# Kernel tuning notes

Measured on AMD Instinct MI355X. Metric: run time of the kernel, lower is better.

Reference implementation:

```python
import jax, jax.numpy as jnp
import numpy as np

NX = NY = 2048
DT = 0.01
DX = 1.0
DY = 1.0
RE = 1.0
NLEVEL = int(np.log2(NY)) + 1  # 12 levels


def pad_zero(x):
    # Dirichlet (zero) halo of width 1: matches boundary_condition_u/v/k/cw
    return jnp.pad(x, ((0, 0), (0, 0), (1, 1), (1, 1)))


def pad_edge(x):
    # Edge-replicate halo (incl. corners): matches boundary_condition_p
    return jnp.pad(x, ((0, 0), (0, 0), (1, 1), (1, 1)), mode='edge')


def conv2d(x, w, stride=1):
    return jax.lax.conv_general_dilated(
        x, w, (stride, stride), 'VALID',
        dimension_numbers=('NCHW', 'OIHW', 'NCHW'))


def upsample2(x):
    return jnp.repeat(jnp.repeat(x, 2, axis=2), 2, axis=3)


def pg_vector(u, v, pad_u, pad_v, k1, ADx_u, ADy_u, ADx_v, ADy_v, AD2_u, AD2_v, w_diff):
    # Petrov-Galerkin dissipation. pad_u/pad_v are the padded ORIGINAL velocities:
    # the torch code references the global values_uu/values_vv buffers here.
    k_u = 0.25 * DX * jnp.abs(0.5 * DX ** -3 * (jnp.abs(u) * DX + jnp.abs(v) * DY) * AD2_u) \
        / (0.001 + (jnp.abs(ADx_u) * DX ** -3 + jnp.abs(ADy_u) * DX ** -3) / 2.0)
    k_v = 0.25 * DY * jnp.abs(0.5 * DX ** -3 * (jnp.abs(u) * DX + jnp.abs(v) * DY) * AD2_v) \
        / (0.001 + (jnp.abs(ADx_v) * DX ** -3 + jnp.abs(ADy_v) * DX ** -3) / 2.0)
    k_u = jnp.minimum(k_u, k1)
    k_v = jnp.minimum(k_v, k1)
    k_uu = pad_zero(k_u)
    k_vv = pad_zero(k_v)
    k_x = 1.5 * (k_u * AD2_u + conv2d(pad_u * k_uu, w_diff) - u * conv2d(k_uu, w_diff))
    k_y = 1.5 * (k_v * AD2_v + conv2d(pad_v * k_vv, w_diff) - v * conv2d(k_vv, w_diff))
    return k_x, k_y


def f_cycle_mg(pad_u, pad_v, values_p, iteration, w_A, w_res, w_xadv, w_yadv):
    diag = w_A[0, 0, 1, 1]
    b = -(conv2d(pad_u, w_xadv) + conv2d(pad_v, w_yadv)) / DT
    w = jnp.zeros((1, 1, 2, 2), values_p.dtype)
    r = b
    for _ in range(iteration):
        w = jnp.zeros((1, 1, 2, 2), values_p.dtype)
        r = conv2d(pad_edge(values_p), w_A) - b
        r_s = [r]
        for _i in range(1, NLEVEL - 1):
            r = conv2d(r, w_res, stride=2)  # restriction down to 2x2
            r_s.append(r)
        for i in reversed(range(1, NLEVEL - 1)):
            w = w - conv2d(pad_zero(w), w_A) / diag + r_s[i] / diag  # Jacobi smooth
            w = upsample2(w)  # prolongation
        values_p = values_p - w
        values_p = values_p - conv2d(pad_edge(values_p), w_A) / diag + b / diag
    return values_p, w, r


def setup_inputs() -> dict:
    key = jax.random.key(0)
    ku, kv, kp = jax.random.split(key, 3)
    shp = (1, 1, NY, NX)
    f32 = jnp.float32
    values_u = jax.random.normal(ku, shp, f32) * 0.1
    values_v = jax.random.normal(kv, shp, f32) * 0.1
    values_p = jax.random.normal(kp, shp, f32) * 0.1
    Fx = jnp.zeros(shp, f32)
    Fy = jnp.zeros(shp, f32)
    k1 = jnp.ones(shp, f32) * (DX ** 2 / DT)
    # FD stencils (learned conv params in the torch module)
    w_xadv = jnp.array([[0., 0., 0.], [-0.5, 0., 0.5], [0., 0., 0.]], f32).reshape(1, 1, 3, 3) / DX
    w_yadv = jnp.array([[0., -0.5, 0.], [0., 0., 0.], [0., 0.5, 0.]], f32).reshape(1, 1, 3, 3) / DY
    lap = jnp.array([[0., 1., 0.], [1., -4., 1.], [0., 1., 0.]], f32).reshape(1, 1, 3, 3) / DX ** 2
    w_diff = lap
    w_A = lap  # diag = -4
    w_res = jnp.full((1, 1, 2, 2), 0.25, f32)
    return dict(values_u=values_u, values_v=values_v, values_p=values_p,
                Fx=Fx, Fy=Fy, k1=k1,
                w_xadv=w_xadv, w_yadv=w_yadv, w_diff=w_diff, w_A=w_A, w_res=w_res,
                iteration=5)


def reference(values_u, values_v, values_p, Fx, Fy, k1,
              w_xadv, w_yadv, w_diff, w_A, w_res, iteration):
    pad_u = pad_zero(values_u)
    pad_v = pad_zero(values_v)
    pad_p = pad_edge(values_p)
    Grapx_p = conv2d(pad_p, w_xadv) * DT
    Grapy_p = conv2d(pad_p, w_yadv) * DT
    ADx_u = conv2d(pad_u, w_xadv); ADy_u = conv2d(pad_u, w_yadv)
    ADx_v = conv2d(pad_v, w_xadv); ADy_v = conv2d(pad_v, w_yadv)
    AD2_u = conv2d(pad_u, w_diff); AD2_v = conv2d(pad_v, w_diff)
    k_x, k_y = pg_vector(values_u, values_v, pad_u, pad_v, k1,
                         ADx_u, ADy_u, ADx_v, ADy_v, AD2_u, AD2_v, w_diff)
    b_u = values_u + 0.5 * (RE * k_x * DT - values_u * ADx_u * DT - values_v * ADy_u * DT) - Grapx_p - Fx * DT * 0
    b_v = values_v + 0.5 * (RE * k_y * DT - values_u * ADx_v * DT - values_v * ADy_v * DT) - Grapy_p - Fy * DT * 0
    pad_bu = pad_zero(b_u)
    pad_bv = pad_zero(b_v)
    ADx_u = conv2d(pad_bu, w_xadv); ADy_u = conv2d(pad_bu, w_yadv)
    ADx_v = conv2d(pad_bv, w_xadv); ADy_v = conv2d(pad_bv, w_yadv)
    AD2_u = conv2d(pad_bu, w_diff); AD2_v = conv2d(pad_bv, w_diff)
    # torch code closes over the global padded ORIGINAL velocities here (pad_u, pad_v)
    k_x, k_y = pg_vector(b_u, b_v, pad_u, pad_v, k1,
                         ADx_u, ADy_u, ADx_v, ADy_v, AD2_u, AD2_v, w_diff)
    values_u = values_u + RE * k_x * DT - b_u * ADx_u * DT - b_v * ADy_u * DT - Grapx_p - Fx * DT
    values_v = values_v + RE * k_y * DT - b_u * ADx_v * DT - b_v * ADy_v * DT - Grapy_p - Fy * DT
    values_p, w, r = f_cycle_mg(pad_zero(values_u), pad_zero(values_v), values_p,
                                iteration, w_A, w_res, w_xadv, w_yadv)
    pad_p2 = pad_edge(values_p)
    values_u = values_u - conv2d(pad_p2, w_xadv) * DT
    values_v = values_v - conv2d(pad_p2, w_yadv) * DT
    return values_u, values_v, values_p, w, r
```

## Files before the change

### kernel.cpp

```cpp
#include <hip/hip_runtime.h>

#define NN 2048
#define NN2 (NN * NN)

__device__ __forceinline__ void load6z(const float* __restrict__ A, int i, int j0, float a[6]) {
    if ((unsigned)i >= (unsigned)NN) {
#pragma unroll
        for (int q = 0; q < 6; ++q) a[q] = 0.f;
        return;
    }
    const float* row = A + (size_t)i * NN;
    float4 c = *reinterpret_cast<const float4*>(row + j0);
    a[1] = c.x; a[2] = c.y; a[3] = c.z; a[4] = c.w;
    a[0] = (j0 > 0) ? row[j0 - 1] : 0.f;
    a[5] = (j0 + 4 < NN) ? row[j0 + 4] : 0.f;
}
__device__ __forceinline__ void load4z(const float* __restrict__ A, int i, int j0, float a[4]) {
    if ((unsigned)i >= (unsigned)NN) {
#pragma unroll
        for (int q = 0; q < 4; ++q) a[q] = 0.f;
        return;
    }
    float4 c = *reinterpret_cast<const float4*>(A + (size_t)i * NN + j0);
    a[0] = c.x; a[1] = c.y; a[2] = c.z; a[3] = c.w;
}
__device__ __forceinline__ void load6e(const float* __restrict__ A, int i, int j0, float a[6]) {
    i = i < 0 ? 0 : (i > NN - 1 ? NN - 1 : i);
    const float* row = A + (size_t)i * NN;
    float4 c = *reinterpret_cast<const float4*>(row + j0);
    a[1] = c.x; a[2] = c.y; a[3] = c.z; a[4] = c.w;
    a[0] = (j0 > 0) ? row[j0 - 1] : c.x;
    a[5] = (j0 + 4 < NN) ? row[j0 + 4] : c.w;
}
__device__ __forceinline__ void load4e(const float* __restrict__ A, int i, int j0, float a[4]) {
    i = i < 0 ? 0 : (i > NN - 1 ? NN - 1 : i);
    float4 c = *reinterpret_cast<const float4*>(A + (size_t)i * NN + j0);
    a[0] = c.x; a[1] = c.y; a[2] = c.z; a[3] = c.w;
}
__device__ __forceinline__ void store4(float* __restrict__ A, int i, int j0, const float a[4]) {
    *reinterpret_cast<float4*>(A + (size_t)i * NN + j0) = make_float4(a[0], a[1], a[2], a[3]);
}

__global__ __launch_bounds__(256) void k_pred_f(const float* __restrict__ u, const float* __restrict__ v,
                                                const float* __restrict__ k1, const float* __restrict__ p,
                                                float* __restrict__ bu, float* __restrict__ bv) {
    const float DT = 0.01f;
    __shared__ __align__(16) float su[20][72], sv[20][72];
    __shared__ float sku[18][68], skv[18][68];
    const int jb = blockIdx.x * 64;
    const int ib = blockIdx.y * 16;
    const int tid = threadIdx.y * 16 + threadIdx.x;

    for (int idx = tid; idx < 20 * 18; idx += 256) {
        int r = idx / 18, c4 = idx - r * 18;
        int gi = ib - 2 + r;
        int gj = jb - 4 + c4 * 4;
        float4 uu = make_float4(0.f, 0.f, 0.f, 0.f), vv = uu;
        if ((unsigned)gi < (unsigned)NN) {
            if (gj >= 0 && gj + 3 < NN) {
                uu = *reinterpret_cast<const float4*>(u + (size_t)gi * NN + gj);
                vv = *reinterpret_cast<const float4*>(v + (size_t)gi * NN + gj);
            } else {
                float tu[4], tv[4];
#pragma unroll
                for (int q = 0; q < 4; ++q) {
                    int g = gj + q;
                    bool in = (unsigned)g < (unsigned)NN;
                    tu[q] = in ? u[(size_t)gi * NN + g] : 0.f;
                    tv[q] = in ? v[(size_t)gi * NN + g] : 0.f;
                }
                uu = make_float4(tu[0], tu[1], tu[2], tu[3]);
                vv = make_float4(tv[0], tv[1], tv[2], tv[3]);
            }
        }
        *reinterpret_cast<float4*>(&su[r][c4 * 4]) = uu;
        *reinterpret_cast<float4*>(&sv[r][c4 * 4]) = vv;
    }
    __syncthreads();

    for (int idx = tid; idx < 18 * 66; idx += 256) {
        int r = idx / 66, c = idx - r * 66;
        int gi = ib - 1 + r, gj = jb - 1 + c;
        float kuo = 0.f, kvo = 0.f;
        if ((unsigned)gi < (unsigned)NN && (unsigned)gj < (unsigned)NN) {
            int lr = r + 1, lc = c + 3;
            float uc = su[lr][lc], ul = su[lr][lc - 1], ur = su[lr][lc + 1], ut = su[lr - 1][lc], ub = su[lr + 1][lc];
            float vc = sv[lr][lc], vl = sv[lr][lc - 1], vr = sv[lr][lc + 1], vt = sv[lr - 1][lc], vb = sv[lr + 1][lc];
            float ADxu = 0.5f * (ur - ul), ADyu = 0.5f * (ub - ut);
            float ADxv = 0.5f * (vr - vl), ADyv = 0.5f * (vb - vt);
            float Lu = ul + ur + ut + ub - 4.f * uc;
            float Lv = vl + vr + vt + vb - 4.f * vc;
            float s = fabsf(uc) + fabsf(vc);
            float kuv = 0.25f * fabsf(0.5f * s * Lu) / (0.001f + 0.5f * (fabsf(ADxu) + fabsf(ADyu)));
            float kvv = 0.25f * fabsf(0.5f * s * Lv) / (0.001f + 0.5f * (fabsf(ADxv) + fabsf(ADyv)));
            float k1c = k1[(size_t)gi * NN + gj];
            kuo = fminf(kuv, k1c);
            kvo = fminf(kvv, k1c);
        }
        sku[r][c] = kuo;
        skv[r][c] = kvo;
    }
    __syncthreads();

    const int i = ib + threadIdx.y;
    const int j0 = jb + threadIdx.x * 4;
    float p6[6], pu[4], pd[4], obu[4], obv[4];
    load6e(p, i, j0, p6); load4e(p, i - 1, j0, pu); load4e(p, i + 1, j0, pd);
    const int lur = threadIdx.y + 2, lkr = threadIdx.y + 1;
#pragma unroll
    for (int c = 0; c < 4; ++c) {
        int luc = threadIdx.x * 4 + c + 4, lkc = threadIdx.x * 4 + c + 1;
        float uc = su[lur][luc], ul = su[lur][luc - 1], ur = su[lur][luc + 1], ut = su[lur - 1][luc], ub = su[lur + 1][luc];
        float vc = sv[lur][luc], vl = sv[lur][luc - 1], vr = sv[lur][luc + 1], vt = sv[lur - 1][luc], vb = sv[lur + 1][luc];
        float kuc = sku[lkr][lkc], kul = sku[lkr][lkc - 1], kur = sku[lkr][lkc + 1], kut = sku[lkr - 1][lkc], kub = sku[lkr + 1][lkc];
        float kvc = skv[lkr][lkc], kvl = skv[lkr][lkc - 1], kvr = skv[lkr][lkc + 1], kvt = skv[lkr - 1][lkc], kvb = skv[lkr + 1][lkc];
        float ADxu = 0.5f * (ur - ul), ADyu = 0.5f * (ub - ut);
        float ADxv = 0.5f * (vr - vl), ADyv = 0.5f * (vb - vt);
        float Lu = ul + ur + ut + ub - 4.f * uc;
        float Lv = vl + vr + vt + vb - 4.f * vc;
        float Lku = kul + kur + kut + kub - 4.f * kuc;
        float Lkv = kvl + kvr + kvt + kvb - 4.f * kvc;
        float Luku = ul * kul + ur * kur + ut * kut + ub * kub - 4.f * uc * kuc;
        float Lvkv = vl * kvl + vr * kvr + vt * kvt + vb * kvb - 4.f * vc * kvc;
        float kx = 1.5f * (kuc * Lu + Luku - uc * Lku);
        float ky = 1.5f * (kvc * Lv + Lvkv - vc * Lkv);
        float Grapx = 0.5f * (p6[c + 2] - p6[c]) * DT;
        float Grapy = 0.5f * (pd[c] - pu[c]) * DT;
        obu[c] = uc + 0.5f * (kx * DT - uc * ADxu * DT - vc * ADyu * DT) - Grapx;
        obv[c] = vc + 0.5f * (ky * DT - uc * ADxv * DT - vc * ADyv * DT) - Grapy;
    }
    store4(bu, i, j0, obu);
    store4(bv, i, j0, obv);
}

__global__ __launch_bounds__(256) void k_corr_f(const float* __restrict__ u, const float* __restrict__ v,
                                                const float* __restrict__ k1, const float* __restrict__ p,
                                                const float* __restrict__ bu, const float* __restrict__ bv,
                                                const float* __restrict__ Fx, const float* __restrict__ Fy,
                                                float* __restrict__ un, float* __restrict__ vn) {
    const float DT = 0.01f;
    __shared__ __align__(16) float sbu[20][72], sbv[20][72];
    __shared__ float sku[18][68], skv[18][68];
    const int jb = blockIdx.x * 64;
    const int ib = blockIdx.y * 16;
    const int tid = threadIdx.y * 16 + threadIdx.x;

    for (int idx = tid; idx < 20 * 18; idx += 256) {
        int r = idx / 18, c4 = idx - r * 18;
        int gi = ib - 2 + r;
        int gj = jb - 4 + c4 * 4;
        float4 uu = make_float4(0.f, 0.f, 0.f, 0.f), vv = uu;
        if ((unsigned)gi < (unsigned)NN) {
            if (gj >= 0 && gj + 3 < NN) {
                uu = *reinterpret_cast<const float4*>(bu + (size_t)gi * NN + gj);
                vv = *reinterpret_cast<const float4*>(bv + (size_t)gi * NN + gj);
            } else {
                float tu[4], tv[4];
#pragma unroll
                for (int q = 0; q < 4; ++q) {
                    int g = gj + q;
                    bool in = (unsigned)g < (unsigned)NN;
                    tu[q] = in ? bu[(size_t)gi * NN + g] : 0.f;
                    tv[q] = in ? bv[(size_t)gi * NN + g] : 0.f;
                }
                uu = make_float4(tu[0], tu[1], tu[2], tu[3]);
                vv = make_float4(tv[0], tv[1], tv[2], tv[3]);
            }
        }
        *reinterpret_cast<float4*>(&sbu[r][c4 * 4]) = uu;
        *reinterpret_cast<float4*>(&sbv[r][c4 * 4]) = vv;
    }
    __syncthreads();

    for (int idx = tid; idx < 18 * 66; idx += 256) {
        int r = idx / 66, c = idx - r * 66;
        int gi = ib - 1 + r, gj = jb - 1 + c;
        float kuo = 0.f, kvo = 0.f;
        if ((unsigned)gi < (unsigned)NN && (unsigned)gj < (unsigned)NN) {
            int lr = r + 1, lc = c + 3;
            float uc = sbu[lr][lc], ul = sbu[lr][lc - 1], ur = sbu[lr][lc + 1], ut = sbu[lr - 1][lc], ub = sbu[lr + 1][lc];
            float vc = sbv[lr][lc], vl = sbv[lr][lc - 1], vr = sbv[lr][lc + 1], vt = sbv[lr - 1][lc], vb = sbv[lr + 1][lc];
            float ADxu = 0.5f * (ur - ul), ADyu = 0.5f * (ub - ut);
            float ADxv = 0.5f * (vr - vl), ADyv = 0.5f * (vb - vt);
            float Lu = ul + ur + ut + ub - 4.f * uc;
            float Lv = vl + vr + vt + vb - 4.f * vc;
            float s = fabsf(uc) + fabsf(vc);
            float kuv = 0.25f * fabsf(0.5f * s * Lu) / (0.001f + 0.5f * (fabsf(ADxu) + fabsf(ADyu)));
            float kvv = 0.25f * fabsf(0.5f * s * Lv) / (0.001f + 0.5f * (fabsf(ADxv) + fabsf(ADyv)));
            float k1c = k1[(size_t)gi * NN + gj];
            kuo = fminf(kuv, k1c);
            kvo = fminf(kvv, k1c);
        }
        sku[r][c] = kuo;
        skv[r][c] = kvo;
    }
    __syncthreads();

    const int i = ib + threadIdx.y;
    const int j0 = jb + threadIdx.x * 4;
    float p6[6], pu[4], pd[4];
    float u6[6], uu[4], ud[4], v6[6], vu[4], vd[4], fx[4], fy[4], oun[4], ovn[4];
    load6e(p, i, j0, p6); load4e(p, i - 1, j0, pu); load4e(p, i + 1, j0, pd);
    load6z(u, i, j0, u6); load4z(u, i - 1, j0, uu); load4z(u, i + 1, j0, ud);
    load6z(v, i, j0, v6); load4z(v, i - 1, j0, vu); load4z(v, i + 1, j0, vd);
    load4z(Fx, i, j0, fx); load4z(Fy, i, j0, fy);
    const int lbr = threadIdx.y + 2, lkr = threadIdx.y + 1;
#pragma unroll
    for (int c = 0; c < 4; ++c) {
        int lbc = threadIdx.x * 4 + c + 4, lkc = threadIdx.x * 4 + c + 1;
        float buc = sbu[lbr][lbc], bul = sbu[lbr][lbc - 1], bur = sbu[lbr][lbc + 1], but = sbu[lbr - 1][lbc], bub = sbu[lbr + 1][lbc];
        float bvc = sbv[lbr][lbc], bvl = sbv[lbr][lbc - 1], bvr = sbv[lbr][lbc + 1], bvt = sbv[lbr - 1][lbc], bvb = sbv[lbr + 1][lbc];
        float kuc = sku[lkr][lkc], kul = sku[lkr][lkc - 1], kur = sku[lkr][lkc + 1], kut = sku[lkr - 1][lkc], kub = sku[lkr + 1][lkc];
        float kvc = skv[lkr][lkc], kvl = skv[lkr][lkc - 1], kvr = skv[lkr][lkc + 1], kvt = skv[lkr - 1][lkc], kvb = skv[lkr + 1][lkc];
        float uc = u6[c + 1], ul = u6[c], ur = u6[c + 2], ut = uu[c], ub = ud[c];
        float vc = v6[c + 1], vl = v6[c], vr = v6[c + 2], vt = vu[c], vb = vd[c];
        float ADxbu = 0.5f * (bur - bul), ADybu = 0.5f * (bub - but);
        float ADxbv = 0.5f * (bvr - bvl), ADybv = 0.5f * (bvb - bvt);
        float Lbu = bul + bur + but + bub - 4.f * buc;
        float Lbv = bvl + bvr + bvt + bvb - 4.f * bvc;
        float Lku = kul + kur + kut + kub - 4.f * kuc;
        float Lkv = kvl + kvr + kvt + kvb - 4.f * kvc;
        float Luku = ul * kul + ur * kur + ut * kut + ub * kub - 4.f * uc * kuc;
        float Lvkv = vl * kvl + vr * kvr + vt * kvt + vb * kvb - 4.f * vc * kvc;
        float kx = 1.5f * (kuc * Lbu + Luku - buc * Lku);
        float ky = 1.5f * (kvc * Lbv + Lvkv - bvc * Lkv);
        float Grapx = 0.5f * (p6[c + 2] - p6[c]) * DT;
        float Grapy = 0.5f * (pd[c] - pu[c]) * DT;
        oun[c] = uc + kx * DT - buc * ADxbu * DT - bvc * ADybu * DT - Grapx - fx[c] * DT;
        ovn[c] = vc + ky * DT - buc * ADxbv * DT - bvc * ADybv * DT - Grapy - fy[c] * DT;
    }
    store4(un, i, j0, oun);
    store4(vn, i, j0, ovn);
}

__global__ __launch_bounds__(256) void k_rhs_res(const float* __restrict__ un, const float* __restrict__ vn,
                                                 const float* __restrict__ p, float* __restrict__ b,
                                                 float* __restrict__ r1024, float* __restrict__ r512,
                                                 float* __restrict__ r256) {
    __shared__ float s512r[4][64];
    int tx = threadIdx.x, ty = threadIdx.y;
    int jt = blockIdx.x * 64 + tx;
    int it = blockIdx.y * 4 + ty;
    int j0 = jt * 4, i0 = it * 4;
    float bb[4][4];
#pragma unroll
    for (int r = 0; r < 4; ++r) {
        float u6[6], vu[4], vd[4];
        load6z(un, i0 + r, j0, u6);
        load4z(vn, i0 + r - 1, j0, vu);
        load4z(vn, i0 + r + 1, j0, vd);
#pragma unroll
        for (int c = 0; c < 4; ++c)
            bb[r][c] = -100.f * (0.5f * (u6[c + 2] - u6[c]) + 0.5f * (vd[c] - vu[c]));
        store4(b, i0 + r, j0, bb[r]);
    }
    float p6[6][6];
#pragma unroll
    for (int r = 0; r < 6; ++r) load6e(p, i0 - 1 + r, j0, p6[r]);
    float res[4][4];
#pragma unroll
    for (int r = 0; r < 4; ++r)
#pragma unroll
        for (int c = 0; c < 4; ++c) {
            float pc = p6[r + 1][c + 1];
            res[r][c] = p6[r][c + 1] + p6[r + 2][c + 1] + p6[r + 1][c] + p6[r + 1][c + 2] - 4.f * pc - bb[r][c];
        }
    float q00 = 0.25f * (res[0][0] + res[0][1] + res[1][0] + res[1][1]);
    float q01 = 0.25f * (res[0][2] + res[0][3] + res[1][2] + res[1][3]);
    float q10 = 0.25f * (res[2][0] + res[2][1] + res[3][0] + res[3][1]);
    float q11 = 0.25f * (res[2][2] + res[2][3] + res[3][2] + res[3][3]);
    int ci = it * 2, cj = jt * 2;
    *reinterpret_cast<float2*>(r1024 + (size_t)ci * 1024 + cj)       = make_float2(q00, q01);
    *reinterpret_cast<float2*>(r1024 + (size_t)(ci + 1) * 1024 + cj) = make_float2(q10, q11);
    float s = 0.25f * (q00 + q01 + q10 + q11);
    r512[(size_t)it * 512 + jt] = s;
    s512r[ty][tx] = s;
    __syncthreads();
    int tid = ty * 64 + tx;
    if (tid < 64) {
        int a = tid >> 5, c = tid & 31;
        float m = 0.25f * (s512r[2 * a][2 * c] + s512r[2 * a][2 * c + 1] + s512r[2 * a + 1][2 * c] + s512r[2 * a + 1][2 * c + 1]);
        r256[(size_t)(blockIdx.y * 2 + a) * 256 + blockIdx.x * 32 + c] = m;
    }
}

__global__ __launch_bounds__(1024) void k_small2(const float* __restrict__ r256in,
                                                 float* __restrict__ r128g,
                                                 float* __restrict__ w128_out,
                                                 float* __restrict__ r2_out) {
    __shared__ float sr128[128 * 128];
    __shared__ float sr64[64 * 64];
    __shared__ float sr32[32 * 32];
// ... 32 lines not shown
    }
    __syncthreads();
    if (t < 64) {
        int i = t >> 3, j = t & 7;
        const float* s0 = sr16 + (2 * i) * 16 + 2 * j;
        sr8[t] = 0.25f * (s0[0] + s0[1] + s0[16] + s0[17]);
    }
    __syncthreads();
    if (t < 16) {
        int i = t >> 2, j = t & 3;
        const float* s0 = sr8 + (2 * i) * 8 + 2 * j;
        sr4[t] = 0.25f * (s0[0] + s0[1] + s0[8] + s0[9]);
    }
    __syncthreads();
    if (t < 4) {
        int i = t >> 1, j = t & 1;
        const float* s0 = sr4 + (2 * i) * 4 + 2 * j;
        sr2[t] = 0.25f * (s0[0] + s0[1] + s0[4] + s0[5]);
        r2_out[t] = sr2[t];
        float ws = -0.25f * sr2[t];
        wa[(2 * i) * 4 + 2 * j] = ws;
        wa[(2 * i) * 4 + 2 * j + 1] = ws;
        wa[(2 * i + 1) * 4 + 2 * j] = ws;
        wa[(2 * i + 1) * 4 + 2 * j + 1] = ws;
    }
    __syncthreads();

    auto step = [&](const float* win, const float* rl, float* wout, int s) {
        for (int idx = t; idx < s * s; idx += 1024) {
            int i = idx / s, j = idx - i * s;
            float up = i > 0 ? win[(i - 1) * s + j] : 0.f;
            float dn = i < s - 1 ? win[(i + 1) * s + j] : 0.f;
            float lf = j > 0 ? win[i * s + j - 1] : 0.f;
            float rt = j < s - 1 ? win[i * s + j + 1] : 0.f;
            float ws = 0.25f * (up + dn + lf + rt - rl[idx]);
            int o = 2 * s;
            wout[(2 * i) * o + 2 * j] = ws;
            wout[(2 * i) * o + 2 * j + 1] = ws;
            wout[(2 * i + 1) * o + 2 * j] = ws;
            wout[(2 * i + 1) * o + 2 * j + 1] = ws;
        }
    };
    step(wa, sr4, wb, 4);
    __syncthreads();
    step(wb, sr8, wa, 8);
    __syncthreads();
    step(wa, sr16, wb, 16);
    __syncthreads();
    step(wb, sr32, wa, 32);
    __syncthreads();
    step(wa, sr64, w128_out, 64);
}

__global__ __launch_bounds__(256) void k_prolong2(const float* __restrict__ w128, const float* __restrict__ r128,
                                                  const float* __restrict__ r256, float* __restrict__ w512) {
    __shared__ float sw[5][68];
    __shared__ float s128[3][66];
    __shared__ float s256[2][128];
    const int jb = blockIdx.x * 256;
    const int ob = blockIdx.y * 4;
    const int by = blockIdx.y;
    const int rw = by - 2, cw = jb / 4 - 2;
    const int rs = by - 1, cs = jb / 4 - 1;
    const int tid = threadIdx.y * 64 + threadIdx.x;

    for (int idx = tid; idx < 5 * 68; idx += 256) {
        int r = idx / 68, c = idx - r * 68;
        int x = rw + r, y = cw + c;
        sw[r][c] = ((unsigned)x < 128u && (unsigned)y < 128u) ? w128[x * 128 + y] : 0.f;
    }
    __syncthreads();
    if (tid < 3 * 66) {
        int r = tid / 66, c = tid - (tid / 66) * 66;
        int x = rs + r, y = cs + c;
        float val = 0.f;
        if ((unsigned)x < 128u && (unsigned)y < 128u) {
            int lr = r + 1, lc = c + 1;
            val = 0.25f * (sw[lr - 1][lc] + sw[lr + 1][lc] + sw[lr][lc - 1] + sw[lr][lc + 1] - r128[x * 128 + y]);
        }
        s128[r][c] = val;
    }
    __syncthreads();
    {
        int rr = tid >> 7, cc = tid & 127;
        int X = 2 * by + rr, Y = jb / 2 + cc;
        float s = 0.f;
        if (X > 0)   s += s128[((X - 1) >> 1) - rs][(Y >> 1) - cs];
        if (X < 255) s += s128[((X + 1) >> 1) - rs][(Y >> 1) - cs];
        if (Y > 0)   s += s128[(X >> 1) - rs][((Y - 1) >> 1) - cs];
        if (Y < 255) s += s128[(X >> 1) - rs][((Y + 1) >> 1) - cs];
        s256[rr][cc] = 0.25f * (s - r256[X * 256 + Y]);
    }
    __syncthreads();
    const int i = ob + threadIdx.y;
    const int j0 = jb + threadIdx.x * 4;
    const int lr = (i >> 1) - 2 * by;
    float o[4];
#pragma unroll
    for (int c = 0; c < 4; ++c) o[c] = s256[lr][((j0 + c) >> 1) - jb / 2];
    *reinterpret_cast<float4*>(w512 + (size_t)i * 512 + j0) = make_float4(o[0], o[1], o[2], o[3]);
}

template <bool LAST>
__global__ __launch_bounds__(256) void k_pupd3(
    const float* __restrict__ p, const float* __restrict__ b,
    const float* __restrict__ w512, const float* __restrict__ r512,
    const float* __restrict__ r1024,
    float* __restrict__ pdst,
    float* __restrict__ o1024, float* __restrict__ o512, float* __restrict__ o256,
    float* __restrict__ wout, float* __restrict__ un, float* __restrict__ vn)
{
    __shared__ float sW[6][38];
    __shared__ float sS[4][36];
    __shared__ float ws[6][68];
    __shared__ __align__(16) float pmid[12][136];
    __shared__ float pnew[10][130];
    __shared__ float sq[4][64];
    __shared__ float red[2][32];

    const int jb = blockIdx.x * 128;
    const int ib = blockIdx.y * 8;
    const int tid = threadIdx.y * 32 + threadIdx.x;
    const int r1 = ib / 2 - 1, c1 = jb / 2 - 2;
    const int r2 = ib / 4 - 1, c2 = jb / 4 - 2;
    const int r3 = ib / 4 - 2, c3 = jb / 4 - 3;

    for (int idx = tid; idx < 6 * 38; idx += 256) {
        int r = idx / 38, c = idx - r * 38;
        int x = r3 + r, y = c3 + c;
        sW[r][c] = ((unsigned)x < 512u && (unsigned)y < 512u) ? w512[(size_t)x * 512 + y] : 0.f;
    }
    __syncthreads();
    if (tid < 4 * 36) {
        int r = tid / 36, c = tid - (tid / 36) * 36;
        int x = r2 + r, y = c2 + c;
        float val = 0.f;
        if ((unsigned)x < 512u && (unsigned)y < 512u) {
            int lr = r + 1, lc = c + 1;
            val = 0.25f * (sW[lr - 1][lc] + sW[lr + 1][lc] + sW[lr][lc - 1] + sW[lr][lc + 1]
                           - r512[(size_t)x * 512 + y]);
        }
        sS[r][c] = val;
    }
    __syncthreads();
    for (int idx = tid; idx < 6 * 68; idx += 256) {
        int r = idx / 68, c = idx - r * 68;
        int x = r1 + r, y = c1 + c;
        float val = 0.f;
        if ((unsigned)x < 1024u && (unsigned)y < 1024u) {
            float s = 0.f;
            if (x > 0)    s += sS[((x - 1) >> 1) - r2][(y >> 1) - c2];
            if (x < 1023) s += sS[((x + 1) >> 1) - r2][(y >> 1) - c2];
            if (y > 0)    s += sS[(x >> 1) - r2][((y - 1) >> 1) - c2];
            if (y < 1023) s += sS[(x >> 1) - r2][((y + 1) >> 1) - c2];
            val = 0.25f * (s - r1024[(size_t)x * 1024 + y]);
        }
        ws[r][c] = val;
    }
    __syncthreads();
    for (int idx = tid; idx < 12 * 34; idx += 256) {
        int r = idx / 34, q = idx - r * 34;
        int gi = ib - 2 + r;
        int gj0 = jb - 4 + q * 4;
        float vals[4] = {0.f, 0.f, 0.f, 0.f};
        if ((unsigned)gi < (unsigned)NN) {
            if (gj0 >= 0 && gj0 + 3 < NN) {
                float4 pv = *reinterpret_cast<const float4*>(p + (size_t)gi * NN + gj0);
                vals[0] = pv.x; vals[1] = pv.y; vals[2] = pv.z; vals[3] = pv.w;
            } else {
#pragma unroll
                for (int q4 = 0; q4 < 4; ++q4) {
                    int gj = gj0 + q4;
                    vals[q4] = ((unsigned)gj < (unsigned)NN) ? p[(size_t)gi * NN + gj] : 0.f;
                }
            }
        }
#pragma unroll
        for (int q4 = 0; q4 < 4; ++q4) {
            int gj = gj0 + q4;
            float m = 0.f;
            if ((unsigned)gi < (unsigned)NN && (unsigned)gj < (unsigned)NN &&
                gj >= jb - 2 && gj <= jb + 129) {
                m = vals[q4] - ws[(gi >> 1) - r1][(gj >> 1) - c1];
            }
            pmid[r][q * 4 + q4] = m;
        }
    }
    __syncthreads();
    for (int idx = tid; idx < 10 * 130; idx += 256) {
        int r = idx / 130, c = idx - r * 130;
        int gi = ib - 1 + r, gj = jb - 1 + c;
        float val = 0.f;
        if ((unsigned)gi < (unsigned)NN && (unsigned)gj < (unsigned)NN) {
// ... 12 lines not shown
    const int i  = ib + threadIdx.y;
    const int j0 = jb + threadIdx.x * 4;
    const int lr = i - (ib - 1);
    const int lc = j0 - (jb - 1);
    *reinterpret_cast<float4*>(pdst + (size_t)i * NN + j0) =
        make_float4(pnew[lr][lc], pnew[lr][lc + 1], pnew[lr][lc + 2], pnew[lr][lc + 3]);

    if (LAST) {
        const float DT = 0.01f;
        float ow[4];
        int wr = (i >> 1) - r1;
#pragma unroll
        for (int c = 0; c < 4; ++c) ow[c] = ws[wr][((j0 + c) >> 1) - c1];
        store4(wout, i, j0, ow);
        float4 uu = *reinterpret_cast<float4*>(un + (size_t)i * NN + j0);
        float4 vv = *reinterpret_cast<float4*>(vn + (size_t)i * NN + j0);
        float ou[4] = {uu.x, uu.y, uu.z, uu.w};
        float ov[4] = {vv.x, vv.y, vv.z, vv.w};
        int iu = (i > 0 ? i - 1 : 0) - (ib - 1);
        int idn = (i < NN - 1 ? i + 1 : NN - 1) - (ib - 1);
#pragma unroll
        for (int c = 0; c < 4; ++c) {
            int j = j0 + c;
            int jl = (j > 0 ? j - 1 : 0) - (jb - 1);
            int jr = (j < NN - 1 ? j + 1 : NN - 1) - (jb - 1);
            int lcc = j - (jb - 1);
            ou[c] -= 0.5f * (pnew[lr][jr] - pnew[lr][jl]) * DT;
            ov[c] -= 0.5f * (pnew[idn][lcc] - pnew[iu][lcc]) * DT;
        }
        store4(un, i, j0, ou);
        store4(vn, i, j0, ov);
    } else {
        int cr = tid >> 6, cc = tid & 63;
        float q = 0.f;
#pragma unroll
        for (int dr = 0; dr < 2; ++dr) {
#pragma unroll
            for (int dc = 0; dc < 2; ++dc) {
                int i2 = ib + 2 * cr + dr, j2 = jb + 2 * cc + dc;
                int lr2 = i2 - (ib - 1), lc2 = j2 - (jb - 1);
                int iu2 = (i2 > 0 ? i2 - 1 : 0) - (ib - 1);
                int id2 = (i2 < NN - 1 ? i2 + 1 : NN - 1) - (ib - 1);
                int jl2 = (j2 > 0 ? j2 - 1 : 0) - (jb - 1);
                int jr2 = (j2 < NN - 1 ? j2 + 1 : NN - 1) - (jb - 1);
                q += pnew[iu2][lc2] + pnew[id2][lc2] + pnew[lr2][jl2] + pnew[lr2][jr2]
                   - 4.f * pnew[lr2][lc2] - b[(size_t)i2 * NN + j2];
            }
        }
        q *= 0.25f;
        sq[cr][cc] = q;
        o1024[(size_t)(ib / 2 + cr) * 1024 + jb / 2 + cc] = q;
        __syncthreads();
        if (tid < 64) {
            int rr = tid >> 5, c5 = tid & 31;
            float m = 0.25f * (sq[2 * rr][2 * c5] + sq[2 * rr][2 * c5 + 1] +
                               sq[2 * rr + 1][2 * c5] + sq[2 * rr + 1][2 * c5 + 1]);
            o512[(size_t)(ib / 4 + rr) * 512 + jb / 4 + c5] = m;
            red[rr][c5] = m;
        }
        __syncthreads();
        if (tid < 16) {
            float m = 0.25f * (red[0][2 * tid] + red[0][2 * tid + 1] +
                               red[1][2 * tid] + red[1][2 * tid + 1]);
            o256[(size_t)(ib / 8) * 256 + jb / 8 + tid] = m;
        }
    }
}

extern "C" void kernel_launch(void* const* d_in, const int* in_sizes, int n_in,
                              void* d_out, int out_size, void* d_ws, size_t ws_size,
                              hipStream_t stream) {
    const float* u  = (const float*)d_in[0];
    const float* v  = (const float*)d_in[1];
    const float* p  = (const float*)d_in[2];
    const float* Fx = (const float*)d_in[3];
    const float* Fy = (const float*)d_in[4];
    const float* k1 = (const float*)d_in[5];

    float* out = (float*)d_out;
    float* out_u = out;
    float* out_v = out + (size_t)NN2;
    float* out_p = out + 2 * (size_t)NN2;
    float* out_w = out + 3 * (size_t)NN2;
    float* out_r = out + 4 * (size_t)NN2;

    float* wsb = (float*)d_ws;
    float* b  = wsb;
    float* pA = wsb + (size_t)NN2;
    float* pB = wsb + 2 * (size_t)NN2;
    float* base = wsb + 3 * (size_t)NN2;
    float* rA1024 = base;
    float* rA512  = rA1024 + 1024 * 1024;
    float* rA256  = rA512 + 512 * 512;
    float* rB1024 = rA256 + 256 * 256;
    float* rB512  = rB1024 + 1024 * 1024;
    float* rB256  = rB512 + 512 * 512;
    float* r128   = rB256 + 256 * 256;
    float* w128   = r128 + 128 * 128;
    float* w512   = w128 + 128 * 128;

    float* bu = out_w;
    float* bv = out_p;

    dim3 blkT(16, 16);
    dim3 gT(32, 128);
    dim3 blkR(64, 4);
    dim3 gR(8, 128);
    dim3 blkP(32, 8);
    dim3 gP(16, 256);
    dim3 gL(2, 128);

    k_pred_f<<<gT, blkT, 0, stream>>>(u, v, k1, p, bu, bv);
    k_corr_f<<<gT, blkT, 0, stream>>>(u, v, k1, p, bu, bv, Fx, Fy, out_u, out_v);
    k_rhs_res<<<gR, blkR, 0, stream>>>(out_u, out_v, p, b, rA1024, rA512, rA256);

    const float* pcur = p;
    for (int it = 0; it < 5; ++it) {
        const bool useA = (it % 2 == 0);
        const float* R1024 = useA ? rA1024 : rB1024;
        const float* R512  = useA ? rA512  : rB512;
        const float* R256  = useA ? rA256  : rB256;
        float* O1024 = useA ? rB1024 : rA1024;
        float* O512  = useA ? rB512  : rA512;
        float* O256  = useA ? rB256  : rA256;

        k_small2<<<1, 1024, 0, stream>>>(R256, r128, w128, out_r);
        k_prolong2<<<gL, blkR, 0, stream>>>(w128, r128, R256, w512);
        if (it < 4) {
            float* pdst = (it & 1) ? pB : pA;
            k_pupd3<false><<<gP, blkP, 0, stream>>>(pcur, b, w512, R512, R1024,
                                                    pdst, O1024, O512, O256,
                                                    nullptr, nullptr, nullptr);
            pcur = pdst;
        } else {
            k_pupd3<true><<<gP, blkP, 0, stream>>>(pcur, b, w512, R512, R1024,
                                                   out_p, nullptr, nullptr, nullptr,
                                                   out_w, out_u, out_v);
        }
    }
}
```

Measured before the change: 393.1 us.

## Fuse momentum predictor/corrector and fold prolongation into pressure update kernel

Merges the predictor and corrector kernels into one kernel. It recomputes the intermediate b_u/b_v and the k fields on a wider halo in shared memory, so the intermediate no longer makes a global round trip. It also removes the separate 128→256→512 prolongation kernel: each pressure-update block now rebuilds its own w512 tile from w128, r128 and r256 locally. This cuts launches per multigrid iteration and global traffic, at the cost of redundant halo computation, more shared memory per block (possibly lower occupancy), and a few extra barriers. Shared arrays are also padded by one column to reduce bank conflicts.

```diff
diff --git a/kernel.cpp b/kernel.cpp
--- a/kernel.cpp
+++ b/kernel.cpp
@@ -32,58 +32,77 @@
     a[0] = (j0 > 0) ? row[j0 - 1] : c.x;
     a[5] = (j0 + 4 < NN) ? row[j0 + 4] : c.w;
 }
-__device__ __forceinline__ void load4e(const float* __restrict__ A, int i, int j0, float a[4]) {
-    i = i < 0 ? 0 : (i > NN - 1 ? NN - 1 : i);
-    float4 c = *reinterpret_cast<const float4*>(A + (size_t)i * NN + j0);
-    a[0] = c.x; a[1] = c.y; a[2] = c.z; a[3] = c.w;
-}
 __device__ __forceinline__ void store4(float* __restrict__ A, int i, int j0, const float a[4]) {
     *reinterpret_cast<float4*>(A + (size_t)i * NN + j0) = make_float4(a[0], a[1], a[2], a[3]);
 }
 
-__global__ __launch_bounds__(256) void k_pred_f(const float* __restrict__ u, const float* __restrict__ v,
-                                                const float* __restrict__ k1, const float* __restrict__ p,
-                                                float* __restrict__ bu, float* __restrict__ bv) {
+__global__ __launch_bounds__(256) void k_mom(const float* __restrict__ u, const float* __restrict__ v,
+                                             const float* __restrict__ k1, const float* __restrict__ p,
+                                             const float* __restrict__ Fx, const float* __restrict__ Fy,
+                                             float* __restrict__ un, float* __restrict__ vn) {
     const float DT = 0.01f;
-    __shared__ __align__(16) float su[20][72], sv[20][72];
-    __shared__ float sku[18][68], skv[18][68];
+    __shared__ float su[24][73], sv[24][73];
+    __shared__ float sp[22][73];
+    __shared__ float sku[22][71], skv[22][71];
+    __shared__ float sbu[20][69], sbv[20][69];
+    __shared__ float skbu[18][67], skbv[18][67];
     const int jb = blockIdx.x * 64;
     const int ib = blockIdx.y * 16;
     const int tid = threadIdx.y * 16 + threadIdx.x;
 
-    for (int idx = tid; idx < 20 * 18; idx += 256) {
+    for (int idx = tid; idx < 24 * 18; idx += 256) {
         int r = idx / 18, c4 = idx - r * 18;
-        int gi = ib - 2 + r;
+        int gi = ib - 4 + r;
         int gj = jb - 4 + c4 * 4;
-        float4 uu = make_float4(0.f, 0.f, 0.f, 0.f), vv = uu;
+        float tu[4] = {0.f, 0.f, 0.f, 0.f}, tv[4] = {0.f, 0.f, 0.f, 0.f};
         if ((unsigned)gi < (unsigned)NN) {
             if (gj >= 0 && gj + 3 < NN) {
-                uu = *reinterpret_cast<const float4*>(u + (size_t)gi * NN + gj);
-                vv = *reinterpret_cast<const float4*>(v + (size_t)gi * NN + gj);
+                float4 a = *reinterpret_cast<const float4*>(u + (size_t)gi * NN + gj);
+                float4 bq = *reinterpret_cast<const float4*>(v + (size_t)gi * NN + gj);
+                tu[0] = a.x; tu[1] = a.y; tu[2] = a.z; tu[3] = a.w;
+                tv[0] = bq.x; tv[1] = bq.y; tv[2] = bq.z; tv[3] = bq.w;
             } else {
-                float tu[4], tv[4];
 #pragma unroll
                 for (int q = 0; q < 4; ++q) {
                     int g = gj + q;
-                    bool in = (unsigned)g < (unsigned)NN;
-                    tu[q] = in ? u[(size_t)gi * NN + g] : 0.f;
-                    tv[q] = in ? v[(size_t)gi * NN + g] : 0.f;
+                    if ((unsigned)g < (unsigned)NN) {
+                        tu[q] = u[(size_t)gi * NN + g];
+                        tv[q] = v[(size_t)gi * NN + g];
+                    }
                 }
-                uu = make_float4(tu[0], tu[1], tu[2], tu[3]);
-                vv = make_float4(tv[0], tv[1], tv[2], tv[3]);
             }
         }
-        *reinterpret_cast<float4*>(&su[r][c4 * 4]) = uu;
-        *reinterpret_cast<float4*>(&sv[r][c4 * 4]) = vv;
-    }
-    __syncthreads();
-
-    for (int idx = tid; idx < 18 * 66; idx += 256) {
-        int r = idx / 66, c = idx - r * 66;
-        int gi = ib - 1 + r, gj = jb - 1 + c;
+#pragma unroll
+        for (int q = 0; q < 4; ++q) { su[r][c4 * 4 + q] = tu[q]; sv[r][c4 * 4 + q] = tv[q]; }
+    }
+    for (int idx = tid; idx < 22 * 18; idx += 256) {
+        int r = idx / 18, c4 = idx - r * 18;
+        int gi = ib - 3 + r;
+        gi = gi < 0 ? 0 : (gi > NN - 1 ? NN - 1 : gi);
+        int gj = jb - 4 + c4 * 4;
+        float tp[4];
+        if (gj >= 0 && gj + 3 < NN) {
+            float4 a = *reinterpret_cast<const float4*>(p + (size_t)gi * NN + gj);
+            tp[0] = a.x; tp[1] = a.y; tp[2] = a.z; tp[3] = a.w;
+        } else {
+#pragma unroll
+            for (int q = 0; q < 4; ++q) {
+                int g = gj + q;
+                g = g < 0 ? 0 : (g > NN - 1 ? NN - 1 : g);
+                tp[q] = p[(size_t)gi * NN + g];
+            }
+        }
+#pragma unroll
+        for (int q = 0; q < 4; ++q) sp[r][c4 * 4 + q] = tp[q];
+    }
+    __syncthreads();
+
+    for (int idx = tid; idx < 22 * 70; idx += 256) {
+        int r = idx / 70, c = idx - r * 70;
+        int gi = ib - 3 + r, gj = jb - 3 + c;
         float kuo = 0.f, kvo = 0.f;
         if ((unsigned)gi < (unsigned)NN && (unsigned)gj < (unsigned)NN) {
-            int lr = r + 1, lc = c + 3;
+            int lr = r + 1, lc = c + 1;
             float uc = su[lr][lc], ul = su[lr][lc - 1], ur = su[lr][lc + 1], ut = su[lr - 1][lc], ub = su[lr + 1][lc];
             float vc = sv[lr][lc], vl = sv[lr][lc - 1], vr = sv[lr][lc + 1], vt = sv[lr - 1][lc], vb = sv[lr + 1][lc];
             float ADxu = 0.5f * (ur - ul), ADyu = 0.5f * (ub - ut);
@@ -102,73 +121,35 @@
     }
     __syncthreads();
 
-    const int i = ib + threadIdx.y;
-    const int j0 = jb + threadIdx.x * 4;
-    float p6[6], pu[4], pd[4], obu[4], obv[4];
-    load6e(p, i, j0, p6); load4e(p, i - 1, j0, pu); load4e(p, i + 1, j0, pd);
-    const int lur = threadIdx.y + 2, lkr = threadIdx.y + 1;
-#pragma unroll
-    for (int c = 0; c < 4; ++c) {
-        int luc = threadIdx.x * 4 + c + 4, lkc = threadIdx.x * 4 + c + 1;
-        float uc = su[lur][luc], ul = su[lur][luc - 1], ur = su[lur][luc + 1], ut = su[lur - 1][luc], ub = su[lur + 1][luc];
-        float vc = sv[lur][luc], vl = sv[lur][luc - 1], vr = sv[lur][luc + 1], vt = sv[lur - 1][luc], vb = sv[lur + 1][luc];
-        float kuc = sku[lkr][lkc], kul = sku[lkr][lkc - 1], kur = sku[lkr][lkc + 1], kut = sku[lkr - 1][lkc], kub = sku[lkr + 1][lkc];
-        float kvc = skv[lkr][lkc], kvl = skv[lkr][lkc - 1], kvr = skv[lkr][lkc + 1], kvt = skv[lkr - 1][lkc], kvb = skv[lkr + 1][lkc];
-        float ADxu = 0.5f * (ur - ul), ADyu = 0.5f * (ub - ut);
-        float ADxv = 0.5f * (vr - vl), ADyv = 0.5f * (vb - vt);
-        float Lu = ul + ur + ut + ub - 4.f * uc;
-        float Lv = vl + vr + vt + vb - 4.f * vc;
-        float Lku = kul + kur + kut + kub - 4.f * kuc;
-        float Lkv = kvl + kvr + kvt + kvb - 4.f * kvc;
-        float Luku = ul * kul + ur * kur + ut * kut + ub * kub - 4.f * uc * kuc;
-        float Lvkv = vl * kvl + vr * kvr + vt * kvt + vb * kvb - 4.f * vc * kvc;
-        float kx = 1.5f * (kuc * Lu + Luku - uc * Lku);
-        float ky = 1.5f * (kvc * Lv + Lvkv - vc * Lkv);
-        float Grapx = 0.5f * (p6[c + 2] - p6[c]) * DT;
-        float Grapy = 0.5f * (pd[c] - pu[c]) * DT;
-        obu[c] = uc + 0.5f * (kx * DT - uc * ADxu * DT - vc * ADyu * DT) - Grapx;
-        obv[c] = vc + 0.5f * (ky * DT - uc * ADxv * DT - vc * ADyv * DT) - Grapy;
-    }
-    store4(bu, i, j0, obu);
-    store4(bv, i, j0, obv);
-}
-
-__global__ __launch_bounds__(256) void k_corr_f(const float* __restrict__ u, const float* __restrict__ v,
-                                                const float* __restrict__ k1, const float* __restrict__ p,
-                                                const float* __restrict__ bu, const float* __restrict__ bv,
-                                                const float* __restrict__ Fx, const float* __restrict__ Fy,
-                                                float* __restrict__ un, float* __restrict__ vn) {
-    const float DT = 0.01f;
-    __shared__ __align__(16) float sbu[20][72], sbv[20][72];
-    __shared__ float sku[18][68], skv[18][68];
-    const int jb = blockIdx.x * 64;
-    const int ib = blockIdx.y * 16;
-    const int tid = threadIdx.y * 16 + threadIdx.x;
-
-    for (int idx = tid; idx < 20 * 18; idx += 256) {
-        int r = idx / 18, c4 = idx - r * 18;
-        int gi = ib - 2 + r;
-        int gj = jb - 4 + c4 * 4;
-        float4 uu = make_float4(0.f, 0.f, 0.f, 0.f), vv = uu;
-        if ((unsigned)gi < (unsigned)NN) {
-            if (gj >= 0 && gj + 3 < NN) {
-                uu = *reinterpret_cast<const float4*>(bu + (size_t)gi * NN + gj);
-                vv = *reinterpret_cast<const float4*>(bv + (size_t)gi * NN + gj);
-            } else {
-                float tu[4], tv[4];
-#pragma unroll
-                for (int q = 0; q < 4; ++q) {
-                    int g = gj + q;
-                    bool in = (unsigned)g < (unsigned)NN;
-                    tu[q] = in ? bu[(size_t)gi * NN + g] : 0.f;
-                    tv[q] = in ? bv[(size_t)gi * NN + g] : 0.f;
-                }
-                uu = make_float4(tu[0], tu[1], tu[2], tu[3]);
-                vv = make_float4(tv[0], tv[1], tv[2], tv[3]);
-            }
-        }
-        *reinterpret_cast<float4*>(&sbu[r][c4 * 4]) = uu;
-        *reinterpret_cast<float4*>(&sbv[r][c4 * 4]) = vv;
+    for (int idx = tid; idx < 20 * 68; idx += 256) {
+        int r = idx / 68, c = idx - r * 68;
+        int gi = ib - 2 + r, gj = jb - 2 + c;
+        float buo = 0.f, bvo = 0.f;
+        if ((unsigned)gi < (unsigned)NN && (unsigned)gj < (unsigned)NN) {
+            int lu = r + 2, cu = c + 2;
+            int lk = r + 1, ck = c + 1;
+            int lp = r + 1, cp = c + 2;
+            float uc = su[lu][cu], ul = su[lu][cu - 1], ur = su[lu][cu + 1], ut = su[lu - 1][cu], ub = su[lu + 1][cu];
+            float vc = sv[lu][cu], vl = sv[lu][cu - 1], vr = sv[lu][cu + 1], vt = sv[lu - 1][cu], vb = sv[lu + 1][cu];
+            float kuc = sku[lk][ck], kul = sku[lk][ck - 1], kur = sku[lk][ck + 1], kut = sku[lk - 1][ck], kub = sku[lk + 1][ck];
+            float kvc = skv[lk][ck], kvl = skv[lk][ck - 1], kvr = skv[lk][ck + 1], kvt = skv[lk - 1][ck], kvb = skv[lk + 1][ck];
+            float ADxu = 0.5f * (ur - ul), ADyu = 0.5f * (ub - ut);
+            float ADxv = 0.5f * (vr - vl), ADyv = 0.5f * (vb - vt);
+            float Lu = ul + ur + ut + ub - 4.f * uc;
+            float Lv = vl + vr + vt + vb - 4.f * vc;
+            float Lku = kul + kur + kut + kub - 4.f * kuc;
+            float Lkv = kvl + kvr + kvt + kvb - 4.f * kvc;
+            float Luku = ul * kul + ur * kur + ut * kut + ub * kub - 4.f * uc * kuc;
+            float Lvkv = vl * kvl + vr * kvr + vt * kvt + vb * kvb - 4.f * vc * kvc;
+            float kx = 1.5f * (kuc * Lu + Luku - uc * Lku);
+            float ky = 1.5f * (kvc * Lv + Lvkv - vc * Lkv);
+            float Grapx = 0.5f * (sp[lp][cp + 1] - sp[lp][cp - 1]) * DT;
+            float Grapy = 0.5f * (sp[lp + 1][cp] - sp[lp - 1][cp]) * DT;
+            buo = uc + 0.5f * (kx * DT - uc * ADxu * DT - vc * ADyu * DT) - Grapx;
+            bvo = vc + 0.5f * (ky * DT - uc * ADxv * DT - vc * ADyv * DT) - Grapy;
+        }
+        sbu[r][c] = buo;
+        sbv[r][c] = bvo;
     }
     __syncthreads();
 
@@ -177,7 +158,7 @@
         int gi = ib - 1 + r, gj = jb - 1 + c;
         float kuo = 0.f, kvo = 0.f;
         if ((unsigned)gi < (unsigned)NN && (unsigned)gj < (unsigned)NN) {
-            int lr = r + 1, lc = c + 3;
+            int lr = r + 1, lc = c + 1;
             float uc = sbu[lr][lc], ul = sbu[lr][lc - 1], ur = sbu[lr][lc + 1], ut = sbu[lr - 1][lc], ub = sbu[lr + 1][lc];
             float vc = sbv[lr][lc], vl = sbv[lr][lc - 1], vr = sbv[lr][lc + 1], vt = sbv[lr - 1][lc], vb = sbv[lr + 1][lc];
             float ADxu = 0.5f * (ur - ul), ADyu = 0.5f * (ub - ut);
@@ -191,29 +172,30 @@
             kuo = fminf(kuv, k1c);
             kvo = fminf(kvv, k1c);
         }
-        sku[r][c] = kuo;
-        skv[r][c] = kvo;
+        skbu[r][c] = kuo;
+        skbv[r][c] = kvo;
     }
     __syncthreads();
 
     const int i = ib + threadIdx.y;
     const int j0 = jb + threadIdx.x * 4;
-    float p6[6], pu[4], pd[4];
-    float u6[6], uu[4], ud[4], v6[6], vu[4], vd[4], fx[4], fy[4], oun[4], ovn[4];
-    load6e(p, i, j0, p6); load4e(p, i - 1, j0, pu); load4e(p, i + 1, j0, pd);
-    load6z(u, i, j0, u6); load4z(u, i - 1, j0, uu); load4z(u, i + 1, j0, ud);
-    load6z(v, i, j0, v6); load4z(v, i - 1, j0, vu); load4z(v, i + 1, j0, vd);
+    float fx[4], fy[4], oun[4], ovn[4];
     load4z(Fx, i, j0, fx); load4z(Fy, i, j0, fy);
-    const int lbr = threadIdx.y + 2, lkr = threadIdx.y + 1;
+    const int lb = threadIdx.y + 2;
+    const int lk = threadIdx.y + 1;
+    const int lu = threadIdx.y + 4;
+    const int lp = threadIdx.y + 3;
 #pragma unroll
     for (int c = 0; c < 4; ++c) {
-        int lbc = threadIdx.x * 4 + c + 4, lkc = threadIdx.x * 4 + c + 1;
-        float buc = sbu[lbr][lbc], bul = sbu[lbr][lbc - 1], bur = sbu[lbr][lbc + 1], but = sbu[lbr - 1][lbc], bub = sbu[lbr + 1][lbc];
-        float bvc = sbv[lbr][lbc], bvl = sbv[lbr][lbc - 1], bvr = sbv[lbr][lbc + 1], bvt = sbv[lbr - 1][lbc], bvb = sbv[lbr + 1][lbc];
-        float kuc = sku[lkr][lkc], kul = sku[lkr][lkc - 1], kur = sku[lkr][lkc + 1], kut = sku[lkr - 1][lkc], kub = sku[lkr + 1][lkc];
-        float kvc = skv[lkr][lkc], kvl = skv[lkr][lkc - 1], kvr = skv[lkr][lkc + 1], kvt = skv[lkr - 1][lkc], kvb = skv[lkr + 1][lkc];
-        float uc = u6[c + 1], ul = u6[c], ur = u6[c + 2], ut = uu[c], ub = ud[c];
-        float vc = v6[c + 1], vl = v6[c], vr = v6[c + 2], vt = vu[c], vb = vd[c];
+        int cb = threadIdx.x * 4 + c + 2;
+        int ck = threadIdx.x * 4 + c + 1;
+        int cu = threadIdx.x * 4 + c + 4;
+        float buc = sbu[lb][cb], bul = sbu[lb][cb - 1], bur = sbu[lb][cb + 1], but = sbu[lb - 1][cb], bub = sbu[lb + 1][cb];
+        float bvc = sbv[lb][cb], bvl = sbv[lb][cb - 1], bvr = sbv[lb][cb + 1], bvt = sbv[lb - 1][cb], bvb = sbv[lb + 1][cb];
+        float kuc = skbu[lk][ck], kul = skbu[lk][ck - 1], kur = skbu[lk][ck + 1], kut = skbu[lk - 1][ck], kub = skbu[lk + 1][ck];
+        float kvc = skbv[lk][ck], kvl = skbv[lk][ck - 1], kvr = skbv[lk][ck + 1], kvt = skbv[lk - 1][ck], kvb = skbv[lk + 1][ck];
+        float uc = su[lu][cu], ul = su[lu][cu - 1], ur = su[lu][cu + 1], ut = su[lu - 1][cu], ub = su[lu + 1][cu];
+        float vc = sv[lu][cu], vl = sv[lu][cu - 1], vr = sv[lu][cu + 1], vt = sv[lu - 1][cu], vb = sv[lu + 1][cu];
         float ADxbu = 0.5f * (bur - bul), ADybu = 0.5f * (bub - but);
         float ADxbv = 0.5f * (bvr - bvl), ADybv = 0.5f * (bvb - bvt);
         float Lbu = bul + bur + but + bub - 4.f * buc;
@@ -224,8 +206,8 @@
         float Lvkv = vl * kvl + vr * kvr + vt * kvt + vb * kvb - 4.f * vc * kvc;
         float kx = 1.5f * (kuc * Lbu + Luku - buc * Lku);
         float ky = 1.5f * (kvc * Lbv + Lvkv - bvc * Lkv);
-        float Grapx = 0.5f * (p6[c + 2] - p6[c]) * DT;
-        float Grapy = 0.5f * (pd[c] - pu[c]) * DT;
+        float Grapx = 0.5f * (sp[lp][cu + 1] - sp[lp][cu - 1]) * DT;
+        float Grapy = 0.5f * (sp[lp + 1][cu] - sp[lp - 1][cu]) * DT;
         oun[c] = uc + kx * DT - buc * ADxbu * DT - bvc * ADybu * DT - Grapx - fx[c] * DT;
         ovn[c] = vc + ky * DT - buc * ADxbv * DT - bvc * ADybv * DT - Grapy - fy[c] * DT;
     }
@@ -237,7 +219,7 @@
                                                  const float* __restrict__ p, float* __restrict__ b,
                                                  float* __restrict__ r1024, float* __restrict__ r512,
                                                  float* __restrict__ r256) {
-    __shared__ float s512r[4][64];
+    __shared__ float s512r[4][65];
     int tx = threadIdx.x, ty = threadIdx.y;
     int jt = blockIdx.x * 64 + tx;
     int it = blockIdx.y * 4 + ty;
@@ -376,83 +358,70 @@
     step(wa, sr64, w128_out, 64);
 }
 
-__global__ __launch_bounds__(256) void k_prolong2(const float* __restrict__ w128, const float* __restrict__ r128,
-                                                  const float* __restrict__ r256, float* __restrict__ w512) {
-    __shared__ float sw[5][68];
-    __shared__ float s128[3][66];
-    __shared__ float s256[2][128];
-    const int jb = blockIdx.x * 256;
-    const int ob = blockIdx.y * 4;
-    const int by = blockIdx.y;
-    const int rw = by - 2, cw = jb / 4 - 2;
-    const int rs = by - 1, cs = jb / 4 - 1;
-    const int tid = threadIdx.y * 64 + threadIdx.x;
-
-    for (int idx = tid; idx < 5 * 68; idx += 256) {
-        int r = idx / 68, c = idx - r * 68;
-        int x = rw + r, y = cw + c;
-        sw[r][c] = ((unsigned)x < 128u && (unsigned)y < 128u) ? w128[x * 128 + y] : 0.f;
-    }
-    __syncthreads();
-    if (tid < 3 * 66) {
-        int r = tid / 66, c = tid - (tid / 66) * 66;
-        int x = rs + r, y = cs + c;
-        float val = 0.f;
-        if ((unsigned)x < 128u && (unsigned)y < 128u) {
-            int lr = r + 1, lc = c + 1;
-            val = 0.25f * (sw[lr - 1][lc] + sw[lr + 1][lc] + sw[lr][lc - 1] + sw[lr][lc + 1] - r128[x * 128 + y]);
-        }
-        s128[r][c] = val;
-    }
-    __syncthreads();
-    {
-        int rr = tid >> 7, cc = tid & 127;
-        int X = 2 * by + rr, Y = jb / 2 + cc;
-        float s = 0.f;
-        if (X > 0)   s += s128[((X - 1) >> 1) - rs][(Y >> 1) - cs];
-        if (X < 255) s += s128[((X + 1) >> 1) - rs][(Y >> 1) - cs];
-        if (Y > 0)   s += s128[(X >> 1) - rs][((Y - 1) >> 1) - cs];
-        if (Y < 255) s += s128[(X >> 1) - rs][((Y + 1) >> 1) - cs];
-        s256[rr][cc] = 0.25f * (s - r256[X * 256 + Y]);
-    }
-    __syncthreads();
-    const int i = ob + threadIdx.y;
-    const int j0 = jb + threadIdx.x * 4;
-    const int lr = (i >> 1) - 2 * by;
-    float o[4];
-#pragma unroll
-    for (int c = 0; c < 4; ++c) o[c] = s256[lr][((j0 + c) >> 1) - jb / 2];
-    *reinterpret_cast<float4*>(w512 + (size_t)i * 512 + j0) = make_float4(o[0], o[1], o[2], o[3]);
-}
-
 template <bool LAST>
-__global__ __launch_bounds__(256) void k_pupd3(
+__global__ __launch_bounds__(256) void k_pupd4(
     const float* __restrict__ p, const float* __restrict__ b,
-    const float* __restrict__ w512, const float* __restrict__ r512,
+    const float* __restrict__ w128, const float* __restrict__ r128,
+    const float* __restrict__ r256, const float* __restrict__ r512,
     const float* __restrict__ r1024,
     float* __restrict__ pdst,
     float* __restrict__ o1024, float* __restrict__ o512, float* __restrict__ o256,
     float* __restrict__ wout, float* __restrict__ un, float* __restrict__ vn)
 {
-    __shared__ float sW[6][38];
-    __shared__ float sS[4][36];
-    __shared__ float ws[6][68];
-    __shared__ __align__(16) float pmid[12][136];
-    __shared__ float pnew[10][130];
-    __shared__ float sq[4][64];
-    __shared__ float red[2][32];
+    __shared__ float sw[5][15];
+    __shared__ float s128[3][13];
+    __shared__ float s256[3][21];
+    __shared__ float sS[4][37];
+    __shared__ float ws[6][69];
+    __shared__ float pmid[12][137];
+    __shared__ float pnew[10][131];
+    __shared__ float sq[4][65];
+    __shared__ float red[2][33];
 
     const int jb = blockIdx.x * 128;
     const int ib = blockIdx.y * 8;
     const int tid = threadIdx.y * 32 + threadIdx.x;
-    const int r1 = ib / 2 - 1, c1 = jb / 2 - 2;
-    const int r2 = ib / 4 - 1, c2 = jb / 4 - 2;
-    const int r3 = ib / 4 - 2, c3 = jb / 4 - 3;
-
-    for (int idx = tid; idx < 6 * 38; idx += 256) {
-        int r = idx / 38, c = idx - r * 38;
+    const int r1 = ib / 2 - 1,  c1 = jb / 2 - 2;
+    const int r2 = ib / 4 - 1,  c2 = jb / 4 - 2;
+    const int r3 = ib / 8 - 1,  c3 = jb / 8 - 2;
+    const int r4 = ib / 16 - 1, c4 = jb / 16 - 2;
+    const int r5 = ib / 16 - 2, c5 = jb / 16 - 3;
+
+    if (tid < 5 * 14) {
+        int r = tid / 14, c = tid - (tid / 14) * 14;
+        int x = r5 + r, y = c5 + c;
+        sw[r][c] = ((unsigned)x < 128u && (unsigned)y < 128u) ? w128[x * 128 + y] : 0.f;
+    }
+    __syncthreads();
+    if (tid < 3 * 12) {
+        int r = tid / 12, c = tid - (tid / 12) * 12;
+        int x = r4 + r, y = c4 + c;
+        float val = 0.f;
+        if ((unsigned)x < 128u && (unsigned)y < 128u) {
+            int lr = x - r5, lc = y - c5;
+            float s = 0.f;
+            if (x > 0)   s += sw[lr - 1][lc];
+            if (x < 127) s += sw[lr + 1][lc];
+            if (y > 0)   s += sw[lr][lc - 1];
+            if (y < 127) s += sw[lr][lc + 1];
+            val = 0.25f * (s - r128[x * 128 + y]);
+        }
+        s128[r][c] = val;
+    }
+    __syncthreads();
+    if (tid < 3 * 20) {
+        int r = tid / 20, c = tid - (tid / 20) * 20;
         int x = r3 + r, y = c3 + c;
-        sW[r][c] = ((unsigned)x < 512u && (unsigned)y < 512u) ? w512[(size_t)x * 512 + y] : 0.f;
+        float val = 0.f;
+        if ((unsigned)x < 256u && (unsigned)y < 256u) {
+            float s = 0.f;
+            if (x > 0)   s += s128[((x - 1) >> 1) - r4][(y >> 1) - c4];
+            if (x < 255) s += s128[((x + 1) >> 1) - r4][(y >> 1) - c4];
+            if (y > 0)   s += s128[(x >> 1) - r4][((y - 1) >> 1) - c4];
+            if (y < 255) s += s128[(x >> 1) - r4][((y + 1) >> 1) - c4];
+            val = 0.25f * (s - r256[x * 256 + y]);
+        }
+        s256[r][c] = val;
     }
     __syncthreads();
     if (tid < 4 * 36) {
@@ -460,9 +429,12 @@
         int x = r2 + r, y = c2 + c;
         float val = 0.f;
         if ((unsigned)x < 512u && (unsigned)y < 512u) {
-            int lr = r + 1, lc = c + 1;
-            val = 0.25f * (sW[lr - 1][lc] + sW[lr + 1][lc] + sW[lr][lc - 1] + sW[lr][lc + 1]
-                           - r512[(size_t)x * 512 + y]);
+            float s = 0.f;
+            if (x > 0)   s += s256[((x - 1) >> 1) - r3][(y >> 1) - c3];
+            if (x < 511) s += s256[((x + 1) >> 1) - r3][(y >> 1) - c3];
+            if (y > 0)   s += s256[(x >> 1) - r3][((y - 1) >> 1) - c3];
+            if (y < 511) s += s256[(x >> 1) - r3][((y + 1) >> 1) - c3];
+            val = 0.25f * (s - r512[(size_t)x * 512 + y]);
         }
         sS[r][c] = val;
     }
@@ -581,11 +553,11 @@
         o1024[(size_t)(ib / 2 + cr) * 1024 + jb / 2 + cc] = q;
         __syncthreads();
         if (tid < 64) {
-            int rr = tid >> 5, c5 = tid & 31;
-            float m = 0.25f * (sq[2 * rr][2 * c5] + sq[2 * rr][2 * c5 + 1] +
-                               sq[2 * rr + 1][2 * c5] + sq[2 * rr + 1][2 * c5 + 1]);
-            o512[(size_t)(ib / 4 + rr) * 512 + jb / 4 + c5] = m;
-            red[rr][c5] = m;
+            int rr = tid >> 5, c5c = tid & 31;
+            float m = 0.25f * (sq[2 * rr][2 * c5c] + sq[2 * rr][2 * c5c + 1] +
+                               sq[2 * rr + 1][2 * c5c] + sq[2 * rr + 1][2 * c5c + 1]);
+            o512[(size_t)(ib / 4 + rr) * 512 + jb / 4 + c5c] = m;
+            red[rr][c5c] = m;
         }
         __syncthreads();
         if (tid < 16) {
@@ -626,10 +598,6 @@
     float* rB256  = rB512 + 512 * 512;
     float* r128   = rB256 + 256 * 256;
     float* w128   = r128 + 128 * 128;
-    float* w512   = w128 + 128 * 128;
-
-    float* bu = out_w;
-    float* bv = out_p;
 
     dim3 blkT(16, 16);
     dim3 gT(32, 128);
@@ -637,10 +605,8 @@
     dim3 gR(8, 128);
     dim3 blkP(32, 8);
     dim3 gP(16, 256);
-    dim3 gL(2, 128);
-
-    k_pred_f<<<gT, blkT, 0, stream>>>(u, v, k1, p, bu, bv);
-    k_corr_f<<<gT, blkT, 0, stream>>>(u, v, k1, p, bu, bv, Fx, Fy, out_u, out_v);
+
+    k_mom<<<gT, blkT, 0, stream>>>(u, v, k1, p, Fx, Fy, out_u, out_v);
     k_rhs_res<<<gR, blkR, 0, stream>>>(out_u, out_v, p, b, rA1024, rA512, rA256);
 
     const float* pcur = p;
@@ -654,15 +620,14 @@
         float* O256  = useA ? rB256  : rA256;
 
         k_small2<<<1, 1024, 0, stream>>>(R256, r128, w128, out_r);
-        k_prolong2<<<gL, blkR, 0, stream>>>(w128, r128, R256, w512);
         if (it < 4) {
             float* pdst = (it & 1) ? pB : pA;
-            k_pupd3<false><<<gP, blkP, 0, stream>>>(pcur, b, w512, R512, R1024,
+            k_pupd4<false><<<gP, blkP, 0, stream>>>(pcur, b, w128, r128, R256, R512, R1024,
                                                     pdst, O1024, O512, O256,
                                                     nullptr, nullptr, nullptr);
             pcur = pdst;
         } else {
-            k_pupd3<true><<<gP, blkP, 0, stream>>>(pcur, b, w512, R512, R1024,
+            k_pupd4<true><<<gP, blkP, 0, stream>>>(pcur, b, w128, r128, R256, R512, R1024,
                                                    out_p, nullptr, nullptr, nullptr,
                                                    out_w, out_u, out_v);
         }
```

Result: no change. 398.4 us (+1.3%).
